# Performance work log

Hardware: AMD Instinct MI355X
Metric: run time of the kernel (lower is better)

The kernel has to match this reference:

```python
import jax, jax.numpy as jnp
import numpy as np
import math

B, H, L, D = 2, 16, 2048, 64


def setup_inputs() -> dict:
    key = jax.random.key(0)
    kq, kk, kv, km, kb = jax.random.split(key, 5)
    Q = jax.random.normal(kq, (B, H, L, D), dtype=jnp.float32)
    K = jax.random.normal(kk, (B, H, L, D), dtype=jnp.float32)
    V = jax.random.normal(kv, (B, H, L, D), dtype=jnp.float32)
    mask = jax.random.randint(km, (B, 1, L, L), 0, 2, dtype=jnp.int32)
    attn_bias = jax.random.normal(kb, (1, H, L, L), dtype=jnp.float32)
    return {"Q": Q, "K": K, "V": V, "mask": mask, "attn_bias": attn_bias,
            "last_layer_flag": 0}


def reference(Q, K, V, mask, attn_bias, last_layer_flag):
    d_tensor = K.shape[-1]
    # score: [B, H, L, L] = Q @ K^T / sqrt(d)
    score = jnp.einsum("bhqd,bhkd->bhqk", Q, K) / math.sqrt(d_tensor)
    if mask is not None:
        score = jnp.where(mask == 0, jnp.float32(-10000.0), score)
    if attn_bias is not None:
        score = score + attn_bias
    if last_layer_flag:
        return jnp.mean(score, axis=1)  # mean over heads: [B, L, L]
    score = jax.nn.softmax(score, axis=-1)
    out = jnp.einsum("bhqk,bhkd->bhqd", score, V)  # [B, H, L, D]
    return (out, score)
```

## Files before the change

### kernel.cpp

```cpp
#include <hip/hip_runtime.h>
#include <hip/hip_bf16.h>

#define Bb 2
#define Hh 16
#define Ll 2048
#define Dd 64
#define OUT_ELEMS (Bb*Hh*Ll*Dd)
#define NT (Ll/64)

typedef __attribute__((ext_vector_type(8))) short bf16x8;
typedef __attribute__((ext_vector_type(4))) float f32x4;
typedef __attribute__((ext_vector_type(4))) int i32x4;

__device__ __forceinline__ unsigned short f2bf(float f) {
    union { float f; unsigned int u; } a; a.f = f;
    unsigned int r = a.u + 0x7FFFu + ((a.u >> 16) & 1u);
    return (unsigned short)(r >> 16);
}

__device__ __forceinline__ int swz(int row, int colByte) {
    return row * 128 + (colByte ^ ((row & 7) << 4));
}

__global__ __launch_bounds__(256)
void attn_fused(const float* __restrict__ Q, const float* __restrict__ K,
                const float* __restrict__ V, const int* __restrict__ M,
                const float* __restrict__ Bi, float* __restrict__ out)
{
    __shared__ char Ks[64 * 128];
    __shared__ char VTs[64 * 128];
    __shared__ char Ps[64 * 128];

    const int bid = blockIdx.x;
    const int b  = bid & 1;
    const int qt = (bid >> 1) & 31;
    const int h  = bid >> 6;
    const int q0 = qt * 64;

    const int tid  = threadIdx.x;
    const int w    = tid >> 6;
    const int lane = tid & 63;
    const int g    = lane >> 4;
    const int c16  = lane & 15;
    const int qr   = w * 16 + c16;

    const float* Qp = Q  + ((size_t)(b * Hh + h) * Ll + q0) * Dd;
    const float* Kp = K  + (size_t)(b * Hh + h) * Ll * Dd;
    const float* Vp = V  + (size_t)(b * Hh + h) * Ll * Dd;
    const int*   Mp = M  + (size_t)b * Ll * Ll + (size_t)q0 * Ll;
    const float* Bp = Bi + (size_t)h * Ll * Ll + (size_t)q0 * Ll;
    float* Op = out + ((size_t)(b * Hh + h) * Ll + q0) * Dd;
    float* Sp = out + OUT_ELEMS + ((size_t)(b * Hh + h) * Ll + q0) * Ll;

    const size_t ro = (size_t)qr * Ll;

    bf16x8 qf[2];
    {
        const float* qrow = Qp + qr * Dd;
#pragma unroll
        for (int kk = 0; kk < 2; ++kk) {
            f32x4 a = *(const f32x4*)(qrow + kk * 32 + g * 8);
            f32x4 c = *(const f32x4*)(qrow + kk * 32 + g * 8 + 4);
            bf16x8 q8;
            q8[0] = (short)f2bf(a[0]); q8[1] = (short)f2bf(a[1]);
            q8[2] = (short)f2bf(a[2]); q8[3] = (short)f2bf(a[3]);
            q8[4] = (short)f2bf(c[0]); q8[5] = (short)f2bf(c[1]);
            q8[6] = (short)f2bf(c[2]); q8[7] = (short)f2bf(c[3]);
            qf[kk] = q8;
        }
    }

    float4 kreg[4];
    float  vreg[16];
    i32x4  m4[4];
    f32x4  b4[4];

    const int r0 = tid >> 4, d0 = (tid & 15) * 4;

    auto issueK = [&](int k0) {
#pragma unroll
        for (int rep = 0; rep < 4; ++rep)
            kreg[rep] = *(const float4*)(Kp + (size_t)(k0 + r0 + rep * 16) * Dd + d0);
    };
    auto writeK = [&]() {
#pragma unroll
        for (int rep = 0; rep < 4; ++rep) {
            int row = r0 + rep * 16;
            ushort4 u = { f2bf(kreg[rep].x), f2bf(kreg[rep].y),
                          f2bf(kreg[rep].z), f2bf(kreg[rep].w) };
            *(ushort4*)(Ks + swz(row, d0 * 2)) = u;
        }
    };
    auto issueV = [&](int k0) {
#pragma unroll
        for (int r = 0; r < 4; ++r)
#pragma unroll
            for (int i = 0; i < 4; ++i)
                vreg[r * 4 + i] = Vp[(size_t)(k0 + w * 16 + r * 4 + i) * Dd + lane];
    };
    auto writeV = [&]() {
#pragma unroll
        for (int r = 0; r < 4; ++r) {
            ushort4 u = { f2bf(vreg[r * 4 + 0]), f2bf(vreg[r * 4 + 1]),
                          f2bf(vreg[r * 4 + 2]), f2bf(vreg[r * 4 + 3]) };
            *(ushort4*)(VTs + swz(lane, (w * 16 + r * 4) * 2)) = u;
        }
    };
    auto issueMB = [&](int k0) {
#pragma unroll
        for (int ct = 0; ct < 4; ++ct) {
            m4[ct] = *(const i32x4*)(Mp + ro + k0 + ct * 16 + g * 4);
            b4[ct] = *(const f32x4*)(Bp + ro + k0 + ct * 16 + g * 4);
        }
    };

    auto mfmaST = [&](f32x4 (&sacc)[4]) {
#pragma unroll
        for (int kk = 0; kk < 2; ++kk) {
#pragma unroll
            for (int ct = 0; ct < 4; ++ct) {
                bf16x8 af = *(const bf16x8*)(Ks + swz(ct * 16 + c16, kk * 64 + g * 16));
                sacc[ct] = __builtin_amdgcn_mfma_f32_16x16x32_bf16(af, qf[kk], sacc[ct], 0, 0, 0);
            }
        }
    };

    issueK(0);
    issueMB(0);
    float rsv[4] = {0.f, 0.f, 0.f, 0.f};
    for (int t = 0; t < NT; ++t) {
        __syncthreads();
        writeK();
        issueK(((t + 1) & (NT - 1)) * 64);
        __syncthreads();
        f32x4 sacc[4] = {{0,0,0,0},{0,0,0,0},{0,0,0,0},{0,0,0,0}};
        mfmaST(sacc);
#pragma unroll
        for (int ct = 0; ct < 4; ++ct)
#pragma unroll
            for (int r = 0; r < 4; ++r) {
                float s = sacc[ct][r] * 0.125f;
                s = (m4[ct][r] == 0 ? -10000.0f : s) + b4[ct][r];
                rsv[ct] += __expf(s);
            }
        issueMB(((t + 1) & (NT - 1)) * 64);
    }
    float rs = (rsv[0] + rsv[1]) + (rsv[2] + rsv[3]);
    rs += __shfl_xor(rs, 16);
    rs += __shfl_xor(rs, 32);
    const float inv = 1.0f / rs;

    issueV(0);
    f32x4 oacc[4] = {{0,0,0,0},{0,0,0,0},{0,0,0,0},{0,0,0,0}};
    for (int t = 0; t < NT; ++t) {
        __syncthreads();
        writeK();
        writeV();
        issueK(((t + 1) & (NT - 1)) * 64);
        issueV(((t + 1) & (NT - 1)) * 64);
        __syncthreads();
        f32x4 sacc[4] = {{0,0,0,0},{0,0,0,0},{0,0,0,0},{0,0,0,0}};
        mfmaST(sacc);
        const int k0 = t * 64;
#pragma unroll
        for (int ct = 0; ct < 4; ++ct) {
            f32x4 p;
#pragma unroll
            for (int r = 0; r < 4; ++r) {
                float s = sacc[ct][r] * 0.125f;
                s = (m4[ct][r] == 0 ? -10000.0f : s) + b4[ct][r];
                p[r] = __expf(s) * inv;
            }
            __builtin_nontemporal_store(p, (f32x4*)(Sp + ro + k0 + ct * 16 + g * 4));
            ushort4 u = { (unsigned short)f2bf(p[0]), (unsigned short)f2bf(p[1]),
                          (unsigned short)f2bf(p[2]), (unsigned short)f2bf(p[3]) };
            *(ushort4*)(Ps + swz(qr, ct * 32 + g * 8)) = u;
        }
        issueMB(((t + 1) & (NT - 1)) * 64);
#pragma unroll
        for (int kk = 0; kk < 2; ++kk) {
            bf16x8 pf = *(const bf16x8*)(Ps + swz(qr, kk * 64 + g * 16));
#pragma unroll
            for (int dt = 0; dt < 4; ++dt) {
                bf16x8 vf = *(const bf16x8*)(VTs + swz(dt * 16 + c16, kk * 64 + g * 16));
                oacc[dt] = __builtin_amdgcn_mfma_f32_16x16x32_bf16(pf, vf, oacc[dt], 0, 0, 0);
            }
        }
    }

#pragma unroll
    for (int dt = 0; dt < 4; ++dt)
#pragma unroll
        for (int r = 0; r < 4; ++r)
            Op[(w * 16 + g * 4 + r) * Dd + dt * 16 + c16] = oacc[dt][r];
}

extern "C" void kernel_launch(void* const* d_in, const int* in_sizes, int n_in,
                              void* d_out, int out_size, void* d_ws, size_t ws_size,
                              hipStream_t stream) {
    const float* Q  = (const float*)d_in[0];
    const float* K  = (const float*)d_in[1];
    const float* V  = (const float*)d_in[2];
    const int*   M  = (const int*)d_in[3];
    const float* Bi = (const float*)d_in[4];
    float* out = (float*)d_out;

    dim3 grid(Bb * Hh * (Ll / 64));
    dim3 block(256);
    attn_fused<<<grid, block, 0, stream>>>(Q, K, V, M, Bi, out);
}
```

Measured before the change: 476.3 us.

## Double-buffer K and V tiles in LDS with one barrier per iteration

Splits the K and V shared-memory tiles into two ping-pong buffers. The next tile is written into the idle buffer while MFMAs read the current one, so each loop iteration needs one __syncthreads instead of two. The aim is to cut barrier stalls and overlap the LDS stores with compute in both the row-sum pass and the output pass. The cost is more LDS per block (about 40KB instead of 24KB), which may limit how many blocks fit on a CU.

```diff
diff --git a/kernel.cpp b/kernel.cpp
--- a/kernel.cpp
+++ b/kernel.cpp
@@ -27,8 +27,8 @@
                 const float* __restrict__ V, const int* __restrict__ M,
                 const float* __restrict__ Bi, float* __restrict__ out)
 {
-    __shared__ char Ks[64 * 128];
-    __shared__ char VTs[64 * 128];
+    __shared__ char Ks[2][64 * 128];
+    __shared__ char VTs[2][64 * 128];
     __shared__ char Ps[64 * 128];
 
     const int bid = blockIdx.x;
@@ -74,7 +74,6 @@
     float  vreg[16];
     i32x4  m4[4];
     f32x4  b4[4];
-
     const int r0 = tid >> 4, d0 = (tid & 15) * 4;
 
     auto issueK = [&](int k0) {
@@ -82,13 +81,13 @@
         for (int rep = 0; rep < 4; ++rep)
             kreg[rep] = *(const float4*)(Kp + (size_t)(k0 + r0 + rep * 16) * Dd + d0);
     };
-    auto writeK = [&]() {
+    auto writeK = [&](char* buf) {
 #pragma unroll
         for (int rep = 0; rep < 4; ++rep) {
             int row = r0 + rep * 16;
             ushort4 u = { f2bf(kreg[rep].x), f2bf(kreg[rep].y),
                           f2bf(kreg[rep].z), f2bf(kreg[rep].w) };
-            *(ushort4*)(Ks + swz(row, d0 * 2)) = u;
+            *(ushort4*)(buf + swz(row, d0 * 2)) = u;
         }
     };
     auto issueV = [&](int k0) {
@@ -98,12 +97,12 @@
             for (int i = 0; i < 4; ++i)
                 vreg[r * 4 + i] = Vp[(size_t)(k0 + w * 16 + r * 4 + i) * Dd + lane];
     };
-    auto writeV = [&]() {
+    auto writeV = [&](char* buf) {
 #pragma unroll
         for (int r = 0; r < 4; ++r) {
             ushort4 u = { f2bf(vreg[r * 4 + 0]), f2bf(vreg[r * 4 + 1]),
                           f2bf(vreg[r * 4 + 2]), f2bf(vreg[r * 4 + 3]) };
-            *(ushort4*)(VTs + swz(lane, (w * 16 + r * 4) * 2)) = u;
+            *(ushort4*)(buf + swz(lane, (w * 16 + r * 4) * 2)) = u;
         }
     };
     auto issueMB = [&](int k0) {
@@ -114,12 +113,12 @@
         }
     };
 
-    auto mfmaST = [&](f32x4 (&sacc)[4]) {
+    auto mfmaST = [&](const char* kbuf, f32x4 (&sacc)[4]) {
 #pragma unroll
         for (int kk = 0; kk < 2; ++kk) {
 #pragma unroll
             for (int ct = 0; ct < 4; ++ct) {
-                bf16x8 af = *(const bf16x8*)(Ks + swz(ct * 16 + c16, kk * 64 + g * 16));
+                bf16x8 af = *(const bf16x8*)(kbuf + swz(ct * 16 + c16, kk * 64 + g * 16));
                 sacc[ct] = __builtin_amdgcn_mfma_f32_16x16x32_bf16(af, qf[kk], sacc[ct], 0, 0, 0);
             }
         }
@@ -127,14 +126,13 @@
 
     issueK(0);
     issueMB(0);
+    writeK(Ks[0]);
+    issueK(64);
+    __syncthreads();
     float rsv[4] = {0.f, 0.f, 0.f, 0.f};
     for (int t = 0; t < NT; ++t) {
-        __syncthreads();
-        writeK();
-        issueK(((t + 1) & (NT - 1)) * 64);
-        __syncthreads();
         f32x4 sacc[4] = {{0,0,0,0},{0,0,0,0},{0,0,0,0},{0,0,0,0}};
-        mfmaST(sacc);
+        mfmaST(Ks[t & 1], sacc);
 #pragma unroll
         for (int ct = 0; ct < 4; ++ct)
 #pragma unroll
@@ -143,7 +141,10 @@
                 s = (m4[ct][r] == 0 ? -10000.0f : s) + b4[ct][r];
                 rsv[ct] += __expf(s);
             }
+        writeK(Ks[(t + 1) & 1]);
+        issueK(((t + 2) & (NT - 1)) * 64);
         issueMB(((t + 1) & (NT - 1)) * 64);
+        __syncthreads();
     }
     float rs = (rsv[0] + rsv[1]) + (rsv[2] + rsv[3]);
     rs += __shfl_xor(rs, 16);
@@ -151,16 +152,14 @@
     const float inv = 1.0f / rs;
 
     issueV(0);
+    writeV(VTs[0]);
+    issueV(64);
+    __syncthreads();
+
     f32x4 oacc[4] = {{0,0,0,0},{0,0,0,0},{0,0,0,0},{0,0,0,0}};
     for (int t = 0; t < NT; ++t) {
-        __syncthreads();
-        writeK();
-        writeV();
-        issueK(((t + 1) & (NT - 1)) * 64);
-        issueV(((t + 1) & (NT - 1)) * 64);
-        __syncthreads();
         f32x4 sacc[4] = {{0,0,0,0},{0,0,0,0},{0,0,0,0},{0,0,0,0}};
-        mfmaST(sacc);
+        mfmaST(Ks[t & 1], sacc);
         const int k0 = t * 64;
 #pragma unroll
         for (int ct = 0; ct < 4; ++ct) {
@@ -176,16 +175,25 @@
                           (unsigned short)f2bf(p[2]), (unsigned short)f2bf(p[3]) };
             *(ushort4*)(Ps + swz(qr, ct * 32 + g * 8)) = u;
         }
-        issueMB(((t + 1) & (NT - 1)) * 64);
 #pragma unroll
         for (int kk = 0; kk < 2; ++kk) {
             bf16x8 pf = *(const bf16x8*)(Ps + swz(qr, kk * 64 + g * 16));
 #pragma unroll
             for (int dt = 0; dt < 4; ++dt) {
-                bf16x8 vf = *(const bf16x8*)(VTs + swz(dt * 16 + c16, kk * 64 + g * 16));
+                bf16x8 vf = *(const bf16x8*)(VTs[t & 1] + swz(dt * 16 + c16, kk * 64 + g * 16));
                 oacc[dt] = __builtin_amdgcn_mfma_f32_16x16x32_bf16(pf, vf, oacc[dt], 0, 0, 0);
             }
         }
+        if (t + 1 < NT) {
+            writeK(Ks[(t + 1) & 1]);
+            writeV(VTs[(t + 1) & 1]);
+            issueMB((t + 1) * 64);
+        }
+        if (t + 2 < NT) {
+            issueK((t + 2) * 64);
+            issueV((t + 2) * 64);
+        }
+        __syncthreads();
     }
 
 #pragma unroll
```

New measurement: 479.6 us. No clear change (+0.7%).
